# Kernel tuning notes

Measured on AMD Instinct MI355X. Metric: run time of the kernel, lower is better.

The kernel has to match this reference:

```python
import jax, jax.numpy as jnp
import numpy as np

S, B, E, H = 2048, 4, 1024, 16
D = E // H


def setup_inputs() -> dict:
    key = jax.random.key(0)
    ks = jax.random.split(key, 12)
    scale = 1.0 / np.sqrt(E)
    inp = {
        "query": jax.random.normal(ks[0], (S, B, E), jnp.float32),
        "key": jax.random.normal(ks[1], (S, B, E), jnp.float32),
        "value": jax.random.normal(ks[2], (S, B, E), jnp.float32),
        # causal mask: True = masked out (matches masked_fill semantics)
        "attn_mask": jnp.triu(jnp.ones((S, S), jnp.bool_), k=1),
        "Wq": jax.random.normal(ks[3], (E, E), jnp.float32) * scale,
        "bq": jax.random.normal(ks[4], (E,), jnp.float32) * scale,
        "Wk": jax.random.normal(ks[5], (E, E), jnp.float32) * scale,
        "bk": jax.random.normal(ks[6], (E,), jnp.float32) * scale,
        "Wv": jax.random.normal(ks[7], (E, E), jnp.float32) * scale,
        "bv": jax.random.normal(ks[8], (E,), jnp.float32) * scale,
        "Wo": jax.random.normal(ks[9], (E, E), jnp.float32) * scale,
        "bo": jax.random.normal(ks[10], (E,), jnp.float32) * scale,
    }
    return inp


def reference(query, key, value, attn_mask, Wq, bq, Wk, bk, Wv, bv, Wo, bo):
    # inputs are [S, B, E]; torch Linear: y = x @ W.T + b
    def proj_heads(x, W, b):
        y = jnp.einsum("sbe,fe->sbf", x, W) + b          # [S,B,E]
        return y.transpose(1, 0, 2).reshape(B, S, H, D).transpose(0, 2, 1, 3)  # [B,H,S,D]

    Q = proj_heads(query, Wq, bq)
    K = proj_heads(key, Wk, bk)
    V = proj_heads(value, Wv, bv)

    scores = jnp.einsum("bhsd,bhtd->bhst", Q, K) / jnp.sqrt(jnp.float32(D))
    scores = jnp.where(attn_mask[None, None, :, :], -jnp.inf, scores)
    probs = jax.nn.softmax(scores, axis=-1)              # dropout p=0 -> identity

    ctx = jnp.einsum("bhst,bhtd->bhsd", probs, V)        # [B,H,S,D]
    ctx = ctx.transpose(0, 2, 1, 3).reshape(B, S, E).transpose(1, 0, 2)  # [S,B,E]

    out = jnp.einsum("sbe,fe->sbf", ctx, Wo) + bo        # [S,B,E]
    attn_map = probs.mean(axis=1)                        # [B,S,S]
    return out, attn_map
```

## Files before the change

kernel.cpp:

```cpp
#include <hip/hip_runtime.h>
#include <stdint.h>

#define S_LEN 2048
#define B_SZ  4
#define E_SZ  1024
#define H_CNT 16
#define D_HD  64

typedef __attribute__((ext_vector_type(4))) float          f32x4;
typedef __attribute__((ext_vector_type(2))) float          f32x2;
typedef __attribute__((ext_vector_type(8))) __bf16         bf16x8;
typedef __attribute__((ext_vector_type(4))) unsigned short u16x4;
typedef __attribute__((ext_vector_type(4))) int            i32x4;
typedef __attribute__((ext_vector_type(2))) int            i32x2;
typedef unsigned short us;

#define QSCALE 0.1803368801111204f

__device__ __forceinline__ us bfu(float f) {
    __bf16 h = (__bf16)f;
    return __builtin_bit_cast(us, h);
}
__device__ __forceinline__ unsigned pk2(float a, float b) {
    return (unsigned)bfu(a) | ((unsigned)bfu(b) << 16);
}
#define EXP2(x) __builtin_amdgcn_exp2f(x)
#define MFMA(a, b, c) __builtin_amdgcn_mfma_f32_16x16x32_bf16((a), (b), (c), 0, 0, 0)

__device__ __forceinline__ void gll16(const void* g, void* l) {
    __builtin_amdgcn_global_load_lds(
        (const __attribute__((address_space(1))) void*)g,
        (__attribute__((address_space(3))) void*)l, 16, 0, 0);
}

__global__ __launch_bounds__(256)
void convert_many(const float* __restrict__ s0, const float* __restrict__ s1,
                  const float* __restrict__ s2, const float* __restrict__ s3,
                  us* __restrict__ d0, us* __restrict__ d1,
                  us* __restrict__ d2, us* __restrict__ d3,
                  float sc0)
{
    const int which = blockIdx.y;
    const float* s = which == 0 ? s0 : which == 1 ? s1 : which == 2 ? s2 : s3;
    us* d = which == 0 ? d0 : which == 1 ? d1 : which == 2 ? d2 : d3;
    const float sc = which == 0 ? sc0 : 1.0f;
    const int i = blockIdx.x * 256 + threadIdx.x;
    f32x4 v = ((const f32x4*)s)[i];
    u16x4 o;
    o.x = bfu(v.x * sc); o.y = bfu(v.y * sc);
    o.z = bfu(v.z * sc); o.w = bfu(v.w * sc);
    ((u16x4*)d)[i] = o;
}

template<bool AF32, bool OUT_QKV>
__global__ __launch_bounds__(256)
void gemm_bt(const void* __restrict__ Ap,
             const us* __restrict__ Bw,
             const float* __restrict__ bias, float bscale,
             void* __restrict__ Outp)
{
    __shared__ us Al[128 * 64];
    __shared__ us Bl[128 * 64];

    const int t    = threadIdx.x;
    const int lane = t & 63;
    const int wave = t >> 6;
    const int lrow = lane & 15;
    const int lk   = lane >> 4;
    const int bm   = (blockIdx.x >> 3) << 7;
    const int bn   = (blockIdx.x & 7) << 7;
    const int wr   = (wave >> 1) << 6;
    const int wc   = (wave & 1) << 6;

    f32x4 acc[4][4];
    #pragma unroll
    for (int i = 0; i < 4; ++i)
        #pragma unroll
        for (int j = 0; j < 4; ++j) acc[i][j] = (f32x4)0.0f;

    for (int k0 = 0; k0 < E_SZ; k0 += 64) {
        __syncthreads();
        #pragma unroll
        for (int j = 0; j < 4; ++j) {
            const int chunk = wave * 4 + j;
            const int r = chunk * 8 + (lane >> 3);
            const int c = (lane & 7) << 3;
            if (AF32) {
                const float* ga = (const float*)Ap + (size_t)(bm + r) * E_SZ + k0 + c;
                f32x4 u0 = *(const f32x4*)ga;
                f32x4 u1 = *(const f32x4*)(ga + 4);
                unsigned w0 = pk2(u0.x, u0.y);
                unsigned w1 = pk2(u0.z, u0.w);
                unsigned w2 = pk2(u1.x, u1.y);
                unsigned w3 = pk2(u1.z, u1.w);
                i32x4 wv; wv.x = (int)w0; wv.y = (int)w1; wv.z = (int)w2; wv.w = (int)w3;
                *(i32x4*)(&Al[chunk * 512 + lane * 8]) = wv;
            } else {
                const us* ga = (const us*)Ap + (size_t)(bm + r) * E_SZ + k0 + c;
                gll16(ga, &Al[chunk * 512]);
            }
            const us* gb = Bw + (size_t)(bn + r) * E_SZ + k0 + c;
            gll16(gb, &Bl[chunk * 512]);
        }
        __syncthreads();
        #pragma unroll
        for (int kk = 0; kk < 2; ++kk) {
            bf16x8 af[4], bfr[4];
            #pragma unroll
            for (int i = 0; i < 4; ++i)
                af[i] = *(const bf16x8*)(&Al[(wr + i*16 + lrow) * 64 + kk*32 + lk*8]);
            #pragma unroll
            for (int j = 0; j < 4; ++j)
                bfr[j] = *(const bf16x8*)(&Bl[(wc + j*16 + lrow) * 64 + kk*32 + lk*8]);
            #pragma unroll
            for (int i = 0; i < 4; ++i)
                #pragma unroll
                for (int j = 0; j < 4; ++j)
                    acc[i][j] = MFMA(af[i], bfr[j], acc[i][j]);
        }
    }

    const int crow = lk << 2;
    #pragma unroll
    for (int i = 0; i < 4; ++i) {
        #pragma unroll
        for (int j = 0; j < 4; ++j) {
            const int n = bn + wc + j*16 + lrow;
            const float bv = bias[n] * bscale;
            #pragma unroll
            for (int r = 0; r < 4; ++r) {
                const int m = bm + wr + i*16 + crow + r;
                const float val = acc[i][j][r] + bv;
                if (OUT_QKV) {
                    const int s = m >> 2, b = m & 3;
                    const int h = n >> 6, d = n & 63;
                    ((us*)Outp)[((size_t)(b*H_CNT + h)*S_LEN + s)*D_HD + d] = bfu(val);
                } else {
                    ((float*)Outp)[(size_t)m * E_SZ + n] = val;
                }
            }
        }
    }
}

__global__ __launch_bounds__(512, 6)
void flash_fwd(const us* __restrict__ Qb,
               const us* __restrict__ Kb,
               const us* __restrict__ Vb,
               us* __restrict__ ctx,
               float* __restrict__ mout,
               float* __restrict__ lout)
{
    __shared__ us Kl[2][64 * 64];
    __shared__ us Vt[2][64 * 72];
    __shared__ us Pl[8][16 * 72];

    const int t    = threadIdx.x;
    const int lane = t & 63, wave = t >> 6;
    const int lrow = lane & 15, lk = lane >> 4;
    const int bh   = blockIdx.x & 63;
    const int qt   = 15 - (blockIdx.x >> 6);
    const int b    = bh >> 4, h = bh & 15;

    const size_t base = (size_t)bh * S_LEN * D_HD;
    const us* Q = Qb + base;
    const us* K = Kb + base;
    const us* V = Vb + base;

    const int qbase = qt * 128 + wave * 16;
    const int myq   = qbase + lrow;
    us* pl = &Pl[wave][0];

    bf16x8 qf[2];
    #pragma unroll
    for (int ks = 0; ks < 2; ++ks)
        qf[ks] = *(const bf16x8*)(Q + (size_t)myq * D_HD + ks*32 + lk*8);

    f32x4 ctxa[4];
    #pragma unroll
    for (int nf = 0; nf < 4; ++nf) ctxa[nf] = (f32x4)0.0f;
    float mst = -__builtin_inff(), lst = 0.0f;

    const int tU  = t & 255;
    const int vp2 = (tU & 31) << 1;
    const int vd8 = (tU >> 5) << 3;

    i32x4 v0, v1;

    #define STAGE_K(kv_, kl_)                                                        \
        if (t < 256) {                                                               \
            _Pragma("unroll")                                                        \
            for (int i_ = 0; i_ < 2; ++i_) {                                         \
                const int row_  = i_*32 + (t >> 3);                                  \
                const int slot_ = (t & 7) ^ (row_ & 7);                              \
                gll16(K + (size_t)((kv_) + row_)*D_HD + slot_*8,                     \
                      (kl_) + i_*2048 + ((t >> 6) << 9));                            \
            }                                                                        \
        }
    #define LOAD_V(kv_)                                                             \
        if (t >= 256) {                                                              \
            const us* vp_ = V + (size_t)((kv_) + vp2)*D_HD + vd8;                    \
            v0 = *(const i32x4*)vp_;                                                 \
            v1 = *(const i32x4*)(vp_ + D_HD);                                        \
        }
    #define WRITE_V(vt_)                                                             \
        if (t >= 256) {                                                              \
            union { i32x4 v; us s[8]; } ua_, ub_; ua_.v = v0; ub_.v = v1;            \
            _Pragma("unroll")                                                        \
            for (int j_ = 0; j_ < 8; ++j_) {                                         \
                unsigned w_ = (unsigned)ua_.s[j_] | ((unsigned)ub_.s[j_] << 16);     \
                *(unsigned*)((vt_) + (vd8 + j_)*72 + vp2) = w_;                      \
            }                                                                        \
        }

    STAGE_K(0, Kl[0]);
    LOAD_V(0);
    WRITE_V(Vt[0]);
    __syncthreads();

    const int kvend = qt*128 + 128;
    int cur = 0;
    for (int kv = 0; kv < kvend; kv += 64) {
        const bool more = (kv + 64) < kvend;
        if (more) {
            STAGE_K(kv + 64, Kl[cur ^ 1]);
            LOAD_V(kv + 64);
        }

        if (kv <= qbase) {
            const us* kl = Kl[cur];
            const us* vt = Vt[cur];
            f32x4 sa[4];
            #pragma unroll
            for (int nf = 0; nf < 4; ++nf) sa[nf] = (f32x4)0.0f;
            #pragma unroll
            for (int ks = 0; ks < 2; ++ks)
                #pragma unroll
                for (int nf = 0; nf < 4; ++nf) {
                    const int key = nf*16 + lrow;
                    bf16x8 kf = *(const bf16x8*)((const char*)kl + (key << 7) +
                                    (((((ks << 2) | lk)) ^ (lrow & 7)) << 4));
                    sa[nf] = MFMA(kf, qf[ks], sa[nf]);
                }
            if (kv + 63 > qbase) {
                #pragma unroll
                for (int nf = 0; nf < 4; ++nf)
                    #pragma unroll
                    for (int r = 0; r < 4; ++r)
                        if (kv + nf*16 + (lk << 2) + r > myq) sa[nf][r] = -__builtin_inff();
            }
            float pmax = sa[0][0];
            #pragma unroll
            for (int nf = 0; nf < 4; ++nf)
                #pragma unroll
                for (int r = 0; r < 4; ++r) pmax = fmaxf(pmax, sa[nf][r]);
            pmax = fmaxf(pmax, __shfl_xor(pmax, 16));
            pmax = fmaxf(pmax, __shfl_xor(pmax, 32));
            const bool skip = __all(pmax <= mst + 8.0f);
            if (!skip) {
                const float mnew  = fmaxf(mst, pmax);
                const float alpha = EXP2(mst - mnew);
                mst = mnew;
                lst *= alpha;
                float ar[4];
                #pragma unroll
                for (int r = 0; r < 4; ++r) ar[r] = __shfl(alpha, (lk << 2) + r);
                #pragma unroll
                for (int nf = 0; nf < 4; ++nf)
                    #pragma unroll
                    for (int r = 0; r < 4; ++r) ctxa[nf][r] *= ar[r];
            }
            float sum = 0.0f;
            #pragma unroll
            for (int nf = 0; nf < 4; ++nf)
                #pragma unroll
                for (int r = 0; r < 4; ++r) {
                    const float p = EXP2(sa[nf][r] - mst);
                    sa[nf][r] = p;
                    sum += p;
                }
            sum += __shfl_xor(sum, 16);
            sum += __shfl_xor(sum, 32);
            lst += sum;
            #pragma unroll
            for (int nf = 0; nf < 4; ++nf) {
                i32x2 dw;
                dw.x = (int)pk2(sa[nf][0], sa[nf][1]);
                dw.y = (int)pk2(sa[nf][2], sa[nf][3]);
                *(i32x2*)(pl + lrow*72 + nf*16 + (lk << 2)) = dw;
            }
            #pragma unroll
            for (int ks = 0; ks < 2; ++ks) {
                bf16x8 pa = *(const bf16x8*)(pl + lrow*72 + ks*32 + lk*8);
                #pragma unroll
                for (int nf = 0; nf < 4; ++nf) {
                    bf16x8 vf = *(const bf16x8*)(vt + (nf*16 + lrow)*72 + ks*32 + lk*8);
                    ctxa[nf] = MFMA(pa, vf, ctxa[nf]);
                }
            }
        }

        if (more) { WRITE_V(Vt[cur ^ 1]); }
        __syncthreads();
        cur ^= 1;
    }

    const float inv = 1.0f / lst;
    float invr[4];
    #pragma unroll
    for (int r = 0; r < 4; ++r) invr[r] = __shfl(inv, (lk << 2) + r);
    #pragma unroll
    for (int nf = 0; nf < 4; ++nf)
        #pragma unroll
        for (int r = 0; r < 4; ++r) {
            const int srow = qbase + (lk << 2) + r;
            const int d    = nf*16 + lrow;
            ctx[((size_t)srow * B_SZ + b) * E_SZ + h*D_HD + d] = bfu(ctxa[nf][r] * invr[r]);
        }
    if (lane < 16) {
        mout[(size_t)bh * S_LEN + myq] = mst;
        lout[(size_t)bh * S_LEN + myq] = inv * 0.0625f;
    }
    #undef STAGE_K
    #undef LOAD_V
    #undef WRITE_V
}

__global__ __launch_bounds__(512, 4)
void attn_map_k(const us* __restrict__ Qb,
                const us* __restrict__ Kb,
                const float* __restrict__ mrows,
                const float* __restrict__ lrows,
                float* __restrict__ map)
{
    const int t  = threadIdx.x;
    const int jt = blockIdx.x & 15;
    const int it = (blockIdx.x >> 4) & 15;
    const int b  = blockIdx.x >> 8;
    float* mt = map + ((size_t)b * S_LEN + it*128) * S_LEN + jt*128;

    if (jt > it) {
        f32x4 z = (f32x4)0.0f;
        #pragma unroll
        for (int i = 0; i < 8; ++i) {
            const int c = i*512 + t;
            *(f32x4*)(mt + (size_t)(c >> 5) * S_LEN + (c & 31) * 4) = z;
        }
        return;
    }

    __shared__ us Ql[128 * 64];
    __shared__ us Kl[128 * 64];
    __shared__ f32x2 Mll[16 * 128];

    const int lane = t & 63, wave = t >> 6;
    const int lrow = lane & 15, lk = lane >> 4;
    const int wr = (wave >> 1) << 5;
    const int wc = (wave & 1) << 6;

    #pragma unroll
    for (int i = 0; i < 4; ++i) {
        const int idx = i*512 + t;
        const int h = idx >> 7, row = idx & 127;
        f32x2 v;
        v.x = mrows[(size_t)(b*H_CNT + h)*S_LEN + it*128 + row];
        v.y = lrows[(size_t)(b*H_CNT + h)*S_LEN + it*128 + row];
        Mll[idx] = v;
    }

    f32x4 pacc[2][4];
    #pragma unroll
    for (int i = 0; i < 2; ++i)
        #pragma unroll
        for (int j = 0; j < 4; ++j) pacc[i][j] = (f32x4)0.0f;

    const int qrow  = it*128;
    const int krow  = jt*128;
    const int srow  = t >> 3;
    const int sslot = t & 7;

    for (int h = 0; h < H_CNT; ++h) {
        const size_t base = (size_t)(b*H_CNT + h) * S_LEN * D_HD;
        const us* Qh = Qb + base + (size_t)qrow * D_HD;
        const us* Kh = Kb + base + (size_t)krow * D_HD;
        __syncthreads();
        #pragma unroll
        for (int i = 0; i < 2; ++i) {
            const int row  = i*64 + srow;
            const int slot = sslot ^ (row & 7);
            gll16(Qh + (size_t)row * D_HD + slot*8, &Ql[i*4096 + ((t >> 6) << 9)]);
            gll16(Kh + (size_t)row * D_HD + slot*8, &Kl[i*4096 + ((t >> 6) << 9)]);
        }
        __syncthreads();

        bf16x8 kf[4][2];
        #pragma unroll
        for (int nf = 0; nf < 4; ++nf)
            #pragma unroll
            for (int ks = 0; ks < 2; ++ks) {
                const int row = wc + nf*16 + lrow;
                kf[nf][ks] = *(const bf16x8*)(&Kl[row*64 + (((ks<<2)|lk) ^ (row&7))*8]);
            }

        #pragma unroll
        for (int mf = 0; mf < 2; ++mf) {
            const int arow = wr + mf*16 + lrow;
            bf16x8 af0 = *(const bf16x8*)(&Ql[arow*64 + ((lk     ) ^ (arow&7))*8]);
            bf16x8 af1 = *(const bf16x8*)(&Ql[arow*64 + ((lk ^ 4 ^ (arow&7)) ^ 4 ^ 4)*8]);
            af1 = *(const bf16x8*)(&Ql[arow*64 + (((4|lk)) ^ (arow&7))*8 ]);
            f32x2 ml[4];
            #pragma unroll
            for (int r = 0; r < 4; ++r)
                ml[r] = Mll[h*128 + wr + mf*16 + (lk << 2) + r];
            #pragma unroll
            for (int nf = 0; nf < 4; ++nf) {
                f32x4 sa = (f32x4)0.0f;
                sa = MFMA(af0, kf[nf][0], sa);
                sa = MFMA(af1, kf[nf][1], sa);
                #pragma unroll
                for (int r = 0; r < 4; ++r)
                    pacc[mf][nf][r] += EXP2(sa[r] - ml[r].x) * ml[r].y;
            }
        }
    }

    #pragma unroll
    for (int mf = 0; mf < 2; ++mf)
        #pragma unroll
        for (int nf = 0; nf < 4; ++nf)
            #pragma unroll
            for (int r = 0; r < 4; ++r) {
                const int row = wr + mf*16 + (lk << 2) + r;
                const int col = wc + nf*16 + lrow;
                float v = pacc[mf][nf][r];
                if (it == jt && col > row) v = 0.0f;
                mt[(size_t)row * S_LEN + col] = v;
            }
}

extern "C" void kernel_launch(void* const* d_in, const int* in_sizes, int n_in,
                              void* d_out, int out_size, void* d_ws, size_t ws_size,
                              hipStream_t stream)
{
    const float* q_in = (const float*)d_in[0];
    const float* k_in = (const float*)d_in[1];
    const float* v_in = (const float*)d_in[2];
    const float* Wq = (const float*)d_in[4];
    const float* bq = (const float*)d_in[5];
    const float* Wk = (const float*)d_in[6];
    const float* bk = (const float*)d_in[7];
    const float* Wv = (const float*)d_in[8];
    const float* bv = (const float*)d_in[9];
    const float* Wo = (const float*)d_in[10];
    const float* bo = (const float*)d_in[11];

    const size_t EE   = (size_t)E_SZ * E_SZ;
    const size_t BHSD = (size_t)B_SZ * H_CNT * S_LEN * D_HD;
    const size_t SBE  = (size_t)S_LEN * B_SZ * E_SZ;

    us* Wqb = (us*)d_ws;
    us* Wkb = Wqb + EE;
    us* Wvb = Wkb + EE;
    us* Wob = Wvb + EE;
    us* base = Wob + EE;

    const size_t need_big = (4*EE + 6*BHSD) * sizeof(us);
    const bool big = ws_size >= need_big;

    us *Aq, *Ak, *Av, *Qb, *Kb, *Vb, *ctx;
    float* ml;
    if (big) {
        Aq = base;       Ak = Aq + BHSD;  Av = Ak + BHSD;
        Qb = Av + BHSD;  Kb = Qb + BHSD;  Vb = Kb + BHSD;
        ctx = Aq;
        ml  = (float*)Ak;
    } else {
        Aq = Ak = Av = nullptr;
        Qb = base;       Kb = Qb + BHSD;  Vb = Kb + BHSD;
        ctx = Vb + BHSD;
        ml  = (float*)(ctx + SBE);
    }
    float* mrows = ml;
    float* lrows = ml + (size_t)B_SZ * H_CNT * S_LEN;

    float* out = (float*)d_out;
    float* map = out + SBE;

    convert_many<<<dim3(1024, 4), 256, 0, stream>>>(Wq, Wk, Wv, Wo, Wqb, Wkb, Wvb, Wob, QSCALE);

    if (big) {
        convert_many<<<dim3(8192, 3), 256, 0, stream>>>(q_in, k_in, v_in, nullptr,
                                                        Aq, Ak, Av, nullptr, 1.0f);
        gemm_bt<false, true><<<512, 256, 0, stream>>>(Aq, Wqb, bq, QSCALE, Qb);
        gemm_bt<false, true><<<512, 256, 0, stream>>>(Ak, Wkb, bk, 1.0f,   Kb);
        gemm_bt<false, true><<<512, 256, 0, stream>>>(Av, Wvb, bv, 1.0f,   Vb);
    } else {
        gemm_bt<true, true><<<512, 256, 0, stream>>>(q_in, Wqb, bq, QSCALE, Qb);
        gemm_bt<true, true><<<512, 256, 0, stream>>>(k_in, Wkb, bk, 1.0f,   Kb);
        gemm_bt<true, true><<<512, 256, 0, stream>>>(v_in, Wvb, bv, 1.0f,   Vb);
    }

    flash_fwd<<<1024, 512, 0, stream>>>(Qb, Kb, Vb, ctx, mrows, lrows);

    gemm_bt<false, false><<<512, 256, 0, stream>>>(ctx, Wob, bo, 1.0f, d_out);

    attn_map_k<<<B_SZ*16*16, 512, 0, stream>>>(Qb, Kb, mrows, lrows, map);
}
```

Measured before the change: 266.2 us.

## Process 32 query rows per wave in flash attention to reuse K/V fragments

Each wave in the flash-attention kernel now handles two 16-row query groups, so a block covers 256 query rows. Every K and V fragment read from LDS feeds two MFMAs instead of one, and the grid is halved. The intent is to cut LDS traffic and K/V staging per query row. The cost is more registers (occupancy bound lowered from 6 to 4), a larger P buffer in shared memory, fewer blocks, and coarser causal load balance. A redundant load in the attention-map kernel is also cleaned up.

```diff
diff --git a/kernel.cpp b/kernel.cpp
--- a/kernel.cpp
+++ b/kernel.cpp
@@ -143,7 +143,7 @@
     }
 }
 
-__global__ __launch_bounds__(512, 6)
+__global__ __launch_bounds__(512, 4)
 void flash_fwd(const us* __restrict__ Qb,
                const us* __restrict__ Kb,
                const us* __restrict__ Vb,
@@ -153,13 +153,13 @@
 {
     __shared__ us Kl[2][64 * 64];
     __shared__ us Vt[2][64 * 72];
-    __shared__ us Pl[8][16 * 72];
+    __shared__ us Pl[8][32 * 72];
 
     const int t    = threadIdx.x;
     const int lane = t & 63, wave = t >> 6;
     const int lrow = lane & 15, lk = lane >> 4;
     const int bh   = blockIdx.x & 63;
-    const int qt   = 15 - (blockIdx.x >> 6);
+    const int qt   = 7 - (blockIdx.x >> 6);
     const int b    = bh >> 4, h = bh & 15;
 
     const size_t base = (size_t)bh * S_LEN * D_HD;
@@ -167,19 +167,24 @@
     const us* K = Kb + base;
     const us* V = Vb + base;
 
-    const int qbase = qt * 128 + wave * 16;
-    const int myq   = qbase + lrow;
+    const int qbase = qt * 256 + wave * 32;
     us* pl = &Pl[wave][0];
 
-    bf16x8 qf[2];
-    #pragma unroll
-    for (int ks = 0; ks < 2; ++ks)
-        qf[ks] = *(const bf16x8*)(Q + (size_t)myq * D_HD + ks*32 + lk*8);
-
-    f32x4 ctxa[4];
-    #pragma unroll
-    for (int nf = 0; nf < 4; ++nf) ctxa[nf] = (f32x4)0.0f;
-    float mst = -__builtin_inff(), lst = 0.0f;
+    bf16x8 qf[2][2];
+    #pragma unroll
+    for (int g = 0; g < 2; ++g)
+        #pragma unroll
+        for (int ks = 0; ks < 2; ++ks)
+            qf[g][ks] = *(const bf16x8*)(Q + (size_t)(qbase + g*16 + lrow)*D_HD + ks*32 + lk*8);
+
+    f32x4 ctxa[2][4];
+    float mst[2], lst[2];
+    #pragma unroll
+    for (int g = 0; g < 2; ++g) {
+        #pragma unroll
+        for (int nf = 0; nf < 4; ++nf) ctxa[g][nf] = (f32x4)0.0f;
+        mst[g] = -__builtin_inff(); lst[g] = 0.0f;
+    }
 
     const int tU  = t & 255;
     const int vp2 = (tU & 31) << 1;
@@ -218,7 +223,7 @@
     WRITE_V(Vt[0]);
     __syncthreads();
 
-    const int kvend = qt*128 + 128;
+    const int kvend = qt*256 + 256;
     int cur = 0;
     for (int kv = 0; kv < kvend; kv += 64) {
         const bool more = (kv + 64) < kvend;
@@ -227,12 +232,14 @@
             LOAD_V(kv + 64);
         }
 
-        if (kv <= qbase) {
+        if (kv < qbase + 32) {
             const us* kl = Kl[cur];
             const us* vt = Vt[cur];
-            f32x4 sa[4];
-            #pragma unroll
-            for (int nf = 0; nf < 4; ++nf) sa[nf] = (f32x4)0.0f;
+            f32x4 sa[2][4];
+            #pragma unroll
+            for (int g = 0; g < 2; ++g)
+                #pragma unroll
+                for (int nf = 0; nf < 4; ++nf) sa[g][nf] = (f32x4)0.0f;
             #pragma unroll
             for (int ks = 0; ks < 2; ++ks)
                 #pragma unroll
@@ -240,62 +247,69 @@
                     const int key = nf*16 + lrow;
                     bf16x8 kf = *(const bf16x8*)((const char*)kl + (key << 7) +
                                     (((((ks << 2) | lk)) ^ (lrow & 7)) << 4));
-                    sa[nf] = MFMA(kf, qf[ks], sa[nf]);
+                    sa[0][nf] = MFMA(kf, qf[0][ks], sa[0][nf]);
+                    sa[1][nf] = MFMA(kf, qf[1][ks], sa[1][nf]);
                 }
-            if (kv + 63 > qbase) {
+            #pragma unroll
+            for (int g = 0; g < 2; ++g) {
+                const int myq = qbase + g*16 + lrow;
+                if (kv + 63 > qbase + g*16) {
+                    #pragma unroll
+                    for (int nf = 0; nf < 4; ++nf)
+                        #pragma unroll
+                        for (int r = 0; r < 4; ++r)
+                            if (kv + nf*16 + (lk << 2) + r > myq) sa[g][nf][r] = -__builtin_inff();
+                }
+                float pmax = sa[g][0][0];
                 #pragma unroll
                 for (int nf = 0; nf < 4; ++nf)
                     #pragma unroll
-                    for (int r = 0; r < 4; ++r)
-                        if (kv + nf*16 + (lk << 2) + r > myq) sa[nf][r] = -__builtin_inff();
-            }
-            float pmax = sa[0][0];
-            #pragma unroll
-            for (int nf = 0; nf < 4; ++nf)
-                #pragma unroll
-                for (int r = 0; r < 4; ++r) pmax = fmaxf(pmax, sa[nf][r]);
-            pmax = fmaxf(pmax, __shfl_xor(pmax, 16));
-            pmax = fmaxf(pmax, __shfl_xor(pmax, 32));
-            const bool skip = __all(pmax <= mst + 8.0f);
-            if (!skip) {
-                const float mnew  = fmaxf(mst, pmax);
-                const float alpha = EXP2(mst - mnew);
-                mst = mnew;
-                lst *= alpha;
-                float ar[4];
-                #pragma unroll
-                for (int r = 0; r < 4; ++r) ar[r] = __shfl(alpha, (lk << 2) + r);
+                    for (int r = 0; r < 4; ++r) pmax = fmaxf(pmax, sa[g][nf][r]);
+                pmax = fmaxf(pmax, __shfl_xor(pmax, 16));
+                pmax = fmaxf(pmax, __shfl_xor(pmax, 32));
+                const bool skip = __all(pmax <= mst[g] + 8.0f);
+                if (!skip) {
+                    const float mnew  = fmaxf(mst[g], pmax);
+                    const float alpha = EXP2(mst[g] - mnew);
+                    mst[g] = mnew;
+                    lst[g] *= alpha;
+                    float ar[4];
+                    #pragma unroll
+                    for (int r = 0; r < 4; ++r) ar[r] = __shfl(alpha, (lk << 2) + r);
+                    #pragma unroll
+                    for (int nf = 0; nf < 4; ++nf)
+                        #pragma unroll
+                        for (int r = 0; r < 4; ++r) ctxa[g][nf][r] *= ar[r];
+                }
+                float sum = 0.0f;
                 #pragma unroll
                 for (int nf = 0; nf < 4; ++nf)
                     #pragma unroll
-                    for (int r = 0; r < 4; ++r) ctxa[nf][r] *= ar[r];
-            }
-            float sum = 0.0f;
-            #pragma unroll
-            for (int nf = 0; nf < 4; ++nf)
-                #pragma unroll
-                for (int r = 0; r < 4; ++r) {
-                    const float p = EXP2(sa[nf][r] - mst);
-                    sa[nf][r] = p;
-                    sum += p;
+                    for (int r = 0; r < 4; ++r) {
+                        const float p = EXP2(sa[g][nf][r] - mst[g]);
+                        sa[g][nf][r] = p;
+                        sum += p;
+                    }
+                sum += __shfl_xor(sum, 16);
+                sum += __shfl_xor(sum, 32);
+                lst[g] += sum;
+                #pragma unroll
+                for (int nf = 0; nf < 4; ++nf) {
+                    i32x2 dw;
+                    dw.x = (int)pk2(sa[g][nf][0], sa[g][nf][1]);
+                    dw.y = (int)pk2(sa[g][nf][2], sa[g][nf][3]);
+                    *(i32x2*)(pl + (g*16 + lrow)*72 + nf*16 + (lk << 2)) = dw;
                 }
-            sum += __shfl_xor(sum, 16);
-            sum += __shfl_xor(sum, 32);
-            lst += sum;
-            #pragma unroll
-            for (int nf = 0; nf < 4; ++nf) {
-                i32x2 dw;
-                dw.x = (int)pk2(sa[nf][0], sa[nf][1]);
-                dw.y = (int)pk2(sa[nf][2], sa[nf][3]);
-                *(i32x2*)(pl + lrow*72 + nf*16 + (lk << 2)) = dw;
             }
             #pragma unroll
             for (int ks = 0; ks < 2; ++ks) {
-                bf16x8 pa = *(const bf16x8*)(pl + lrow*72 + ks*32 + lk*8);
+                bf16x8 pa0 = *(const bf16x8*)(pl + lrow*72 + ks*32 + lk*8);
+                bf16x8 pa1 = *(const bf16x8*)(pl + (16 + lrow)*72 + ks*32 + lk*8);
                 #pragma unroll
                 for (int nf = 0; nf < 4; ++nf) {
                     bf16x8 vf = *(const bf16x8*)(vt + (nf*16 + lrow)*72 + ks*32 + lk*8);
-                    ctxa[nf] = MFMA(pa, vf, ctxa[nf]);
+                    ctxa[0][nf] = MFMA(pa0, vf, ctxa[0][nf]);
+                    ctxa[1][nf] = MFMA(pa1, vf, ctxa[1][nf]);
                 }
             }
         }
@@ -305,21 +319,25 @@
         cur ^= 1;
     }
 
-    const float inv = 1.0f / lst;
-    float invr[4];
-    #pragma unroll
-    for (int r = 0; r < 4; ++r) invr[r] = __shfl(inv, (lk << 2) + r);
-    #pragma unroll
-    for (int nf = 0; nf < 4; ++nf)
-        #pragma unroll
-        for (int r = 0; r < 4; ++r) {
-            const int srow = qbase + (lk << 2) + r;
-            const int d    = nf*16 + lrow;
-            ctx[((size_t)srow * B_SZ + b) * E_SZ + h*D_HD + d] = bfu(ctxa[nf][r] * invr[r]);
-        }
-    if (lane < 16) {
-        mout[(size_t)bh * S_LEN + myq] = mst;
-        lout[(size_t)bh * S_LEN + myq] = inv * 0.0625f;
+    #pragma unroll
+    for (int g = 0; g < 2; ++g) {
+        const float inv = 1.0f / lst[g];
+        float invr[4];
+        #pragma unroll
+        for (int r = 0; r < 4; ++r) invr[r] = __shfl(inv, (lk << 2) + r);
+        #pragma unroll
+        for (int nf = 0; nf < 4; ++nf)
+            #pragma unroll
+            for (int r = 0; r < 4; ++r) {
+                const int srow = qbase + g*16 + (lk << 2) + r;
+                const int d    = nf*16 + lrow;
+                ctx[((size_t)srow * B_SZ + b) * E_SZ + h*D_HD + d] = bfu(ctxa[g][nf][r] * invr[r]);
+            }
+        if (lane < 16) {
+            const int myq = qbase + g*16 + lrow;
+            mout[(size_t)bh * S_LEN + myq] = mst[g];
+            lout[(size_t)bh * S_LEN + myq] = inv * 0.0625f;
+        }
     }
     #undef STAGE_K
     #undef LOAD_V
@@ -405,9 +423,8 @@
         #pragma unroll
         for (int mf = 0; mf < 2; ++mf) {
             const int arow = wr + mf*16 + lrow;
-            bf16x8 af0 = *(const bf16x8*)(&Ql[arow*64 + ((lk     ) ^ (arow&7))*8]);
-            bf16x8 af1 = *(const bf16x8*)(&Ql[arow*64 + ((lk ^ 4 ^ (arow&7)) ^ 4 ^ 4)*8]);
-            af1 = *(const bf16x8*)(&Ql[arow*64 + (((4|lk)) ^ (arow&7))*8 ]);
+            bf16x8 af0 = *(const bf16x8*)(&Ql[arow*64 + ((lk)     ^ (arow&7))*8]);
+            bf16x8 af1 = *(const bf16x8*)(&Ql[arow*64 + ((4 | lk) ^ (arow&7))*8]);
             f32x2 ml[4];
             #pragma unroll
             for (int r = 0; r < 4; ++r)
@@ -500,7 +517,7 @@
         gemm_bt<true, true><<<512, 256, 0, stream>>>(v_in, Wvb, bv, 1.0f,   Vb);
     }
 
-    flash_fwd<<<1024, 512, 0, stream>>>(Qb, Kb, Vb, ctx, mrows, lrows);
+    flash_fwd<<<512, 512, 0, stream>>>(Qb, Kb, Vb, ctx, mrows, lrows);
 
     gemm_bt<false, false><<<512, 256, 0, stream>>>(ctx, Wob, bo, 1.0f, d_out);
 
```

Result: slower. 303.1 us (+13.9%).
